# Optimization experiments

Hardware: AMD Instinct MI355X
Metric: run time of the kernel (lower is better)

The kernel has to match this reference:

```python
import jax, jax.numpy as jnp
import numpy as np

B, K, N = 8, 4, 131072
DENSITY = 0.3
NEG_PAD = -1000.0
NEG_IDLE = -1.0e8


def setup_inputs() -> dict:
    rng = np.random.default_rng(0)
    mask_s = rng.random((B, K, N)) < DENSITY  # bool, per-slot variable counts
    mask_a = rng.random((B, K, N)) < DENSITY
    ts = int(mask_s.sum())
    ta = int(mask_a.sum())
    key = jax.random.key(0)
    k1, k2, k3, k4 = jax.random.split(key, 4)
    return {
        "rgb": jax.random.normal(k1, (ts, 3), dtype=jnp.float32),
        "logits_surface": jax.random.normal(k2, (ts, 1), dtype=jnp.float32),
        "logits_air": jax.random.normal(k3, (ta, 1), dtype=jnp.float32),
        "idle_states": (jax.random.uniform(k4, (B, K)) < 0.25).astype(jnp.float32),
        "mask_eval_surface": jnp.asarray(mask_s),
        "mask_eval_air": jnp.asarray(mask_a),
    }


def _expand(mask, values):
    # mask: (B,K,N) bool; values: (total, C) packed in row-major (b,k,n) mask order.
    # Returns (B,K,N,C) where masked positions hold their packed value (others garbage,
    # to be overwritten by the caller's jnp.where). Equivalent to the torch B*K scatter loop.
    m = mask.reshape(-1)
    pos = jnp.cumsum(m.astype(jnp.int32)) - 1  # packed index for each masked slot
    pos = jnp.clip(pos, 0, values.shape[0] - 1)
    return jnp.take(values, pos, axis=0).reshape(mask.shape + (values.shape[-1],))


def reference(rgb, logits_surface, logits_air, idle_states,
              mask_eval_surface, mask_eval_air):
    alive = (1.0 - idle_states)[:, :, None, None]  # (B,K,1,1)
    idle = idle_states[:, :, None, None]
    ms = mask_eval_surface[..., None]  # (B,K,N,1)
    ma = mask_eval_air[..., None]

    rgb_out = jnp.where(ms, _expand(mask_eval_surface, rgb) * alive, 0.0)
    logits_surface_out = jnp.where(
        ms, _expand(mask_eval_surface, logits_surface) * alive + idle * NEG_IDLE, NEG_PAD)
    logits_air_out = jnp.where(
        ma, _expand(mask_eval_air, logits_air) * alive + idle * NEG_IDLE, NEG_PAD)
    return rgb_out, logits_surface_out, logits_air_out
```

## Files before the change

### kernel.cpp

```cpp
#include <hip/hip_runtime.h>
#include <stdint.h>

#define NPER      131072
#define NTOT      4194304LL
#define CHUNK     2048
#define NBLK      2048
#define ROUNDS    8
#define NEG_PAD   (-1000.0f)
#define NEG_IDLE  (-100000000.0f)

__global__ __launch_bounds__(256) void count_kernel(
    const int* __restrict__ ms, const int* __restrict__ ma,
    unsigned long long* __restrict__ sums)
{
    long long base = (long long)blockIdx.x * CHUNK;
    const int4* ms4 = (const int4*)(ms + base);
    const int4* ma4 = (const int4*)(ma + base);
    int t = threadIdx.x;
    int4 s0 = ms4[2 * t], s1 = ms4[2 * t + 1];
    int4 a0 = ma4[2 * t], a1 = ma4[2 * t + 1];
    unsigned cs = (s0.x != 0) + (s0.y != 0) + (s0.z != 0) + (s0.w != 0)
                + (s1.x != 0) + (s1.y != 0) + (s1.z != 0) + (s1.w != 0);
    unsigned ca = (a0.x != 0) + (a0.y != 0) + (a0.z != 0) + (a0.w != 0)
                + (a1.x != 0) + (a1.y != 0) + (a1.z != 0) + (a1.w != 0);
    unsigned packed = cs | (ca << 16);
    #pragma unroll
    for (int off = 32; off > 0; off >>= 1)
        packed += __shfl_down(packed, off, 64);
    __shared__ unsigned lds[4];
    int lane = t & 63, wave = t >> 6;
    if (lane == 0) lds[wave] = packed;
    __syncthreads();
    if (t == 0) {
        unsigned tot = lds[0] + lds[1] + lds[2] + lds[3];
        sums[blockIdx.x] = (unsigned long long)(tot & 0xffffu)
                         | ((unsigned long long)(tot >> 16) << 32);
    }
}

__global__ __launch_bounds__(1024) void scan_kernel(unsigned long long* __restrict__ sums)
{
    __shared__ unsigned long long lds[1024];
    int t = threadIdx.x;
    unsigned long long v0 = sums[2 * t], v1 = sums[2 * t + 1];
    unsigned long long pair = v0 + v1;
    unsigned long long x = pair;
    lds[t] = x;
    __syncthreads();
    for (int off = 1; off < 1024; off <<= 1) {
        unsigned long long y = (t >= off) ? lds[t - off] : 0ULL;
        __syncthreads();
        x += y;
        lds[t] = x;
        __syncthreads();
    }
    unsigned long long excl = x - pair;
    sums[2 * t]     = excl;
    sums[2 * t + 1] = excl + v0;
}

__global__ __launch_bounds__(256) void write_kernel(
    const float* __restrict__ rgb, const float* __restrict__ lsurf,
    const float* __restrict__ lair, const float* __restrict__ idle,
    const int* __restrict__ ms, const int* __restrict__ ma,
    const unsigned long long* __restrict__ offs,
    unsigned ts_max, unsigned ta_max,
    float* __restrict__ out_rgb, float* __restrict__ out_ls, float* __restrict__ out_la)
{
    __shared__ unsigned wsum[4];
    long long base = (long long)blockIdx.x * CHUNK;
    int bk = (int)(base >> 17);
    float idle_v    = idle[bk];
    float alive     = 1.0f - idle_v;
    float idle_term = idle_v * NEG_IDLE;
    unsigned long long off64 = offs[blockIdx.x];
    unsigned baseS = (unsigned)(off64 & 0xffffffffULL);
    unsigned baseA = (unsigned)(off64 >> 32);
    int lane = threadIdx.x & 63, wave = threadIdx.x >> 6;

    for (int r = 0; r < ROUNDS; ++r) {
        long long i = base + (long long)r * 256 + threadIdx.x;
        unsigned s = (ms[i] != 0) ? 1u : 0u;
        unsigned a = (ma[i] != 0) ? 1u : 0u;
        unsigned packed = s | (a << 16);
        unsigned x = packed;
        #pragma unroll
        for (int off = 1; off < 64; off <<= 1) {
            unsigned y = __shfl_up(x, off, 64);
            if (lane >= off) x += y;
        }
        if (lane == 63) wsum[wave] = x;
        __syncthreads();
        unsigned w0 = wsum[0], w1 = wsum[1], w2 = wsum[2], w3 = wsum[3];
        __syncthreads();
        unsigned pre  = (wave > 0 ? w0 : 0u) + (wave > 1 ? w1 : 0u) + (wave > 2 ? w2 : 0u);
        unsigned excl = pre + x - packed;
        unsigned total = w0 + w1 + w2 + w3;
        unsigned ps = min(baseS + (excl & 0xffffu), ts_max);
        unsigned pa = min(baseA + (excl >> 16),     ta_max);

        float r0 = 0.f, r1 = 0.f, r2 = 0.f, lso = NEG_PAD, lao = NEG_PAD;
        if (s) {
            r0  = rgb[3 * (long long)ps]     * alive;
            r1  = rgb[3 * (long long)ps + 1] * alive;
            r2  = rgb[3 * (long long)ps + 2] * alive;
            lso = lsurf[ps] * alive + idle_term;
        }
        if (a) lao = lair[pa] * alive + idle_term;

        long long i3 = i * 3;
        out_rgb[i3]     = r0;
        out_rgb[i3 + 1] = r1;
        out_rgb[i3 + 2] = r2;
        out_ls[i] = lso;
        out_la[i] = lao;

        baseS += total & 0xffffu;
        baseA += total >> 16;
    }
}

extern "C" void kernel_launch(void* const* d_in, const int* in_sizes, int n_in,
                              void* d_out, int out_size, void* d_ws, size_t ws_size,
                              hipStream_t stream)
{
    const float* rgb   = (const float*)d_in[0];
    const float* lsurf = (const float*)d_in[1];
    const float* lair  = (const float*)d_in[2];
    const float* idle  = (const float*)d_in[3];
    const int*   ms    = (const int*)d_in[4];
    const int*   ma    = (const int*)d_in[5];

    unsigned ts_max = (unsigned)(in_sizes[1] - 1);
    unsigned ta_max = (unsigned)(in_sizes[2] - 1);

    float* out     = (float*)d_out;
    float* out_rgb = out;
    float* out_ls  = out + NTOT * 3;
    float* out_la  = out_ls + NTOT;

    unsigned long long* sums = (unsigned long long*)d_ws;

    count_kernel<<<NBLK, 256, 0, stream>>>(ms, ma, sums);
    scan_kernel<<<1, 1024, 0, stream>>>(sums);
    write_kernel<<<NBLK, 256, 0, stream>>>(rgb, lsurf, lair, idle, ms, ma, sums,
                                           ts_max, ta_max, out_rgb, out_ls, out_la);
}
```

Measured before the change: 158.5 us.

## Fuse count/scan/write into single-pass decoupled look-back scan kernel

Replaces the three-kernel count, scan and write pipeline with one kernel. Blocks take ordered IDs from an atomic ticket, publish their aggregate and inclusive prefix flags, and compute exclusive offsets by decoupled look-back. Each thread now handles 8 contiguous elements, using bitmasks and popc for the counts, and writes its outputs with vectorized float4 stores. This avoids reading the masks twice and the extra launches, but adds a memset, spin-waiting, and serialization through the look-back chain.

```diff
diff --git a/kernel.cpp b/kernel.cpp
--- a/kernel.cpp
+++ b/kernel.cpp
@@ -5,119 +5,162 @@
 #define NTOT      4194304LL
 #define CHUNK     2048
 #define NBLK      2048
-#define ROUNDS    8
 #define NEG_PAD   (-1000.0f)
 #define NEG_IDLE  (-100000000.0f)
 
-__global__ __launch_bounds__(256) void count_kernel(
-    const int* __restrict__ ms, const int* __restrict__ ma,
-    unsigned long long* __restrict__ sums)
-{
-    long long base = (long long)blockIdx.x * CHUNK;
-    const int4* ms4 = (const int4*)(ms + base);
-    const int4* ma4 = (const int4*)(ma + base);
-    int t = threadIdx.x;
-    int4 s0 = ms4[2 * t], s1 = ms4[2 * t + 1];
-    int4 a0 = ma4[2 * t], a1 = ma4[2 * t + 1];
-    unsigned cs = (s0.x != 0) + (s0.y != 0) + (s0.z != 0) + (s0.w != 0)
-                + (s1.x != 0) + (s1.y != 0) + (s1.z != 0) + (s1.w != 0);
-    unsigned ca = (a0.x != 0) + (a0.y != 0) + (a0.z != 0) + (a0.w != 0)
-                + (a1.x != 0) + (a1.y != 0) + (a1.z != 0) + (a1.w != 0);
-    unsigned packed = cs | (ca << 16);
-    #pragma unroll
-    for (int off = 32; off > 0; off >>= 1)
-        packed += __shfl_down(packed, off, 64);
-    __shared__ unsigned lds[4];
-    int lane = t & 63, wave = t >> 6;
-    if (lane == 0) lds[wave] = packed;
-    __syncthreads();
-    if (t == 0) {
-        unsigned tot = lds[0] + lds[1] + lds[2] + lds[3];
-        sums[blockIdx.x] = (unsigned long long)(tot & 0xffffu)
-                         | ((unsigned long long)(tot >> 16) << 32);
-    }
+typedef unsigned long long u64;
+
+__device__ __forceinline__ u64 ld_acq(const u64* p) {
+    return __hip_atomic_load(p, __ATOMIC_ACQUIRE, __HIP_MEMORY_SCOPE_AGENT);
+}
+__device__ __forceinline__ void st_rel(u64* p, u64 v) {
+    __hip_atomic_store(p, v, __ATOMIC_RELEASE, __HIP_MEMORY_SCOPE_AGENT);
 }
 
-__global__ __launch_bounds__(1024) void scan_kernel(unsigned long long* __restrict__ sums)
-{
-    __shared__ unsigned long long lds[1024];
-    int t = threadIdx.x;
-    unsigned long long v0 = sums[2 * t], v1 = sums[2 * t + 1];
-    unsigned long long pair = v0 + v1;
-    unsigned long long x = pair;
-    lds[t] = x;
-    __syncthreads();
-    for (int off = 1; off < 1024; off <<= 1) {
-        unsigned long long y = (t >= off) ? lds[t - off] : 0ULL;
-        __syncthreads();
-        x += y;
-        lds[t] = x;
-        __syncthreads();
-    }
-    unsigned long long excl = x - pair;
-    sums[2 * t]     = excl;
-    sums[2 * t + 1] = excl + v0;
-}
-
-__global__ __launch_bounds__(256) void write_kernel(
+__global__ __launch_bounds__(256, 4) void fused_expand(
     const float* __restrict__ rgb, const float* __restrict__ lsurf,
     const float* __restrict__ lair, const float* __restrict__ idle,
     const int* __restrict__ ms, const int* __restrict__ ma,
-    const unsigned long long* __restrict__ offs,
-    unsigned ts_max, unsigned ta_max,
+    unsigned rgb_max, unsigned ts_max, unsigned ta_max,
+    unsigned* __restrict__ ticket, u64* __restrict__ flags,
     float* __restrict__ out_rgb, float* __restrict__ out_ls, float* __restrict__ out_la)
 {
+    __shared__ unsigned sh_bid;
     __shared__ unsigned wsum[4];
-    long long base = (long long)blockIdx.x * CHUNK;
-    int bk = (int)(base >> 17);
-    float idle_v    = idle[bk];
-    float alive     = 1.0f - idle_v;
-    float idle_term = idle_v * NEG_IDLE;
-    unsigned long long off64 = offs[blockIdx.x];
-    unsigned baseS = (unsigned)(off64 & 0xffffffffULL);
-    unsigned baseA = (unsigned)(off64 >> 32);
-    int lane = threadIdx.x & 63, wave = threadIdx.x >> 6;
+    __shared__ unsigned sh_exc[2];
+    const int t = threadIdx.x, lane = t & 63, wave = t >> 6;
 
-    for (int r = 0; r < ROUNDS; ++r) {
-        long long i = base + (long long)r * 256 + threadIdx.x;
-        unsigned s = (ms[i] != 0) ? 1u : 0u;
-        unsigned a = (ma[i] != 0) ? 1u : 0u;
-        unsigned packed = s | (a << 16);
-        unsigned x = packed;
-        #pragma unroll
-        for (int off = 1; off < 64; off <<= 1) {
-            unsigned y = __shfl_up(x, off, 64);
-            if (lane >= off) x += y;
+    if (t == 0) sh_bid = atomicAdd(ticket, 1u);
+    __syncthreads();
+    const unsigned bid = sh_bid;
+    const long long base = (long long)bid * CHUNK;
+
+    const int4* ms4 = (const int4*)(ms + base);
+    const int4* ma4 = (const int4*)(ma + base);
+    int4 s0 = ms4[2 * t], s1 = ms4[2 * t + 1];
+    int4 a0 = ma4[2 * t], a1 = ma4[2 * t + 1];
+    unsigned sbits = (unsigned)(s0.x != 0)        | ((unsigned)(s0.y != 0) << 1)
+                   | ((unsigned)(s0.z != 0) << 2) | ((unsigned)(s0.w != 0) << 3)
+                   | ((unsigned)(s1.x != 0) << 4) | ((unsigned)(s1.y != 0) << 5)
+                   | ((unsigned)(s1.z != 0) << 6) | ((unsigned)(s1.w != 0) << 7);
+    unsigned abits = (unsigned)(a0.x != 0)        | ((unsigned)(a0.y != 0) << 1)
+                   | ((unsigned)(a0.z != 0) << 2) | ((unsigned)(a0.w != 0) << 3)
+                   | ((unsigned)(a1.x != 0) << 4) | ((unsigned)(a1.y != 0) << 5)
+                   | ((unsigned)(a1.z != 0) << 6) | ((unsigned)(a1.w != 0) << 7);
+    unsigned cs = __popc(sbits), ca = __popc(abits);
+
+    unsigned cnt = cs | (ca << 16);
+    unsigned x = cnt;
+    #pragma unroll
+    for (int o = 1; o < 64; o <<= 1) {
+        unsigned y = __shfl_up(x, o, 64);
+        if (lane >= o) x += y;
+    }
+    if (lane == 63) wsum[wave] = x;
+    __syncthreads();
+    unsigned w0 = wsum[0], w1 = wsum[1], w2 = wsum[2], w3 = wsum[3];
+    unsigned pre   = (wave > 0 ? w0 : 0u) + (wave > 1 ? w1 : 0u) + (wave > 2 ? w2 : 0u);
+    unsigned tExcl = pre + x - cnt;
+    unsigned tot   = w0 + w1 + w2 + w3;
+    unsigned totS  = tot & 0xffffu, totA = tot >> 16;
+
+    if (bid == 0) {
+        if (t == 0) {
+            st_rel(&flags[0], (u64)totS | ((u64)totA << 24) | (2ULL << 62));
+            sh_exc[0] = 0u; sh_exc[1] = 0u;
         }
-        if (lane == 63) wsum[wave] = x;
-        __syncthreads();
-        unsigned w0 = wsum[0], w1 = wsum[1], w2 = wsum[2], w3 = wsum[3];
-        __syncthreads();
-        unsigned pre  = (wave > 0 ? w0 : 0u) + (wave > 1 ? w1 : 0u) + (wave > 2 ? w2 : 0u);
-        unsigned excl = pre + x - packed;
-        unsigned total = w0 + w1 + w2 + w3;
-        unsigned ps = min(baseS + (excl & 0xffffu), ts_max);
-        unsigned pa = min(baseA + (excl >> 16),     ta_max);
+    } else {
+        if (t == 0)
+            st_rel(&flags[bid], (u64)totS | ((u64)totA << 24) | (1ULL << 62));
+        if (wave == 0) {
+            unsigned accS = 0, accA = 0, off = 0;
+            for (;;) {
+                int idx = (int)bid - 1 - (int)off - lane;
+                u64 w = (idx >= 0) ? ld_acq(&flags[idx]) : (2ULL << 62);
+                int fl = (int)(w >> 62);
+                u64 validm = __ballot(fl != 0);
+                u64 prefm  = __ballot(fl == 2);
+                unsigned vs = (unsigned)(w & 0xffffffu);
+                unsigned va = (unsigned)((w >> 24) & 0xffffffu);
+                if (prefm) {
+                    int p = __ffsll(prefm) - 1;
+                    u64 need = (p >= 63) ? ~0ULL : ((1ULL << (p + 1)) - 1ULL);
+                    if ((validm & need) == need) {
+                        if (lane > p) { vs = 0; va = 0; }
+                        #pragma unroll
+                        for (int o = 32; o; o >>= 1) {
+                            vs += __shfl_down(vs, o, 64);
+                            va += __shfl_down(va, o, 64);
+                        }
+                        accS += __shfl(vs, 0, 64);
+                        accA += __shfl(va, 0, 64);
+                        break;
+                    }
+                } else if (~validm == 0ULL) {
+                    #pragma unroll
+                    for (int o = 32; o; o >>= 1) {
+                        vs += __shfl_down(vs, o, 64);
+                        va += __shfl_down(va, o, 64);
+                    }
+                    accS += __shfl(vs, 0, 64);
+                    accA += __shfl(va, 0, 64);
+                    off += 64;
+                }
+                __builtin_amdgcn_s_sleep(1);
+            }
+            if (lane == 0) {
+                st_rel(&flags[bid],
+                       (u64)(accS + totS) | ((u64)(accA + totA) << 24) | (2ULL << 62));
+                sh_exc[0] = accS; sh_exc[1] = accA;
+            }
+        }
+    }
+    __syncthreads();
+    const unsigned excS = sh_exc[0], excA = sh_exc[1];
 
-        float r0 = 0.f, r1 = 0.f, r2 = 0.f, lso = NEG_PAD, lao = NEG_PAD;
-        if (s) {
-            r0  = rgb[3 * (long long)ps]     * alive;
-            r1  = rgb[3 * (long long)ps + 1] * alive;
-            r2  = rgb[3 * (long long)ps + 2] * alive;
-            lso = lsurf[ps] * alive + idle_term;
+    const int bk = (int)(base >> 17);
+    const float idle_v    = idle[bk];
+    const float alive     = 1.0f - idle_v;
+    const float idle_term = idle_v * NEG_IDLE;
+
+    unsigned rs = excS + (tExcl & 0xffffu);
+    unsigned ra = excA + (tExcl >> 16);
+    const long long e0 = base + 8LL * t;
+
+    float ls_b[8]  __attribute__((aligned(16)));
+    float la_b[8]  __attribute__((aligned(16)));
+    float rg_b[24] __attribute__((aligned(16)));
+    #pragma unroll
+    for (int j = 0; j < 8; ++j) {
+        if ((sbits >> j) & 1u) {
+            unsigned pr = rs < rgb_max ? rs : rgb_max;
+            long long q = 3LL * pr;
+            rg_b[3 * j]     = rgb[q]     * alive;
+            rg_b[3 * j + 1] = rgb[q + 1] * alive;
+            rg_b[3 * j + 2] = rgb[q + 2] * alive;
+            unsigned pl = rs < ts_max ? rs : ts_max;
+            ls_b[j] = lsurf[pl] * alive + idle_term;
+            rs++;
+        } else {
+            rg_b[3 * j] = 0.f; rg_b[3 * j + 1] = 0.f; rg_b[3 * j + 2] = 0.f;
+            ls_b[j] = NEG_PAD;
         }
-        if (a) lao = lair[pa] * alive + idle_term;
+        if ((abits >> j) & 1u) {
+            unsigned pa = ra < ta_max ? ra : ta_max;
+            la_b[j] = lair[pa] * alive + idle_term;
+            ra++;
+        } else {
+            la_b[j] = NEG_PAD;
+        }
+    }
 
-        long long i3 = i * 3;
-        out_rgb[i3]     = r0;
-        out_rgb[i3 + 1] = r1;
-        out_rgb[i3 + 2] = r2;
-        out_ls[i] = lso;
-        out_la[i] = lao;
-
-        baseS += total & 0xffffu;
-        baseA += total >> 16;
-    }
+    float4* ols = (float4*)(out_ls + e0);
+    ols[0] = ((float4*)ls_b)[0]; ols[1] = ((float4*)ls_b)[1];
+    float4* ola = (float4*)(out_la + e0);
+    ola[0] = ((float4*)la_b)[0]; ola[1] = ((float4*)la_b)[1];
+    float4* org = (float4*)(out_rgb + 3 * e0);
+    #pragma unroll
+    for (int q = 0; q < 6; ++q) org[q] = ((float4*)rg_b)[q];
 }
 
 extern "C" void kernel_launch(void* const* d_in, const int* in_sizes, int n_in,
@@ -131,18 +174,21 @@
     const int*   ms    = (const int*)d_in[4];
     const int*   ma    = (const int*)d_in[5];
 
-    unsigned ts_max = (unsigned)(in_sizes[1] - 1);
-    unsigned ta_max = (unsigned)(in_sizes[2] - 1);
+    unsigned rgb_max = (unsigned)(in_sizes[0] / 3 - 1);
+    unsigned ts_max  = (unsigned)(in_sizes[1] - 1);
+    unsigned ta_max  = (unsigned)(in_sizes[2] - 1);
 
     float* out     = (float*)d_out;
     float* out_rgb = out;
     float* out_ls  = out + NTOT * 3;
     float* out_la  = out_ls + NTOT;
 
-    unsigned long long* sums = (unsigned long long*)d_ws;
+    unsigned* ticket = (unsigned*)d_ws;
+    u64* flags = (u64*)((char*)d_ws + 128);
 
-    count_kernel<<<NBLK, 256, 0, stream>>>(ms, ma, sums);
-    scan_kernel<<<1, 1024, 0, stream>>>(sums);
-    write_kernel<<<NBLK, 256, 0, stream>>>(rgb, lsurf, lair, idle, ms, ma, sums,
-                                           ts_max, ta_max, out_rgb, out_ls, out_la);
+    hipMemsetAsync(d_ws, 0, 128 + (size_t)NBLK * 8, stream);
+
+    fused_expand<<<NBLK, 256, 0, stream>>>(rgb, lsurf, lair, idle, ms, ma,
+                                           rgb_max, ts_max, ta_max,
+                                           ticket, flags, out_rgb, out_ls, out_la);
 }
```

After: 402.7 us. +154.0%, slower.
